# Performance work log

Measured on AMD Instinct MI355X. Metric: run time of the kernel, lower is better.

Reference implementation:

```python
import jax, jax.numpy as jnp
import numpy as np

N_NODES = 100000
N_EDGES = 3200000
IN_CH = 256


def setup_inputs() -> dict:
    key = jax.random.key(0)
    ks = jax.random.split(key, 8)
    x = jax.random.normal(ks[0], (N_NODES, IN_CH), dtype=jnp.float32)
    edge_index = jax.random.randint(ks[1], (2, N_EDGES), 0, N_NODES, dtype=jnp.int64)
    alpha = jnp.ones((), dtype=jnp.float32)
    beta = jnp.ones((), dtype=jnp.float32)
    s = 1.0 / np.sqrt(IN_CH)
    W_mlp = jax.random.normal(ks[2], (1, IN_CH), dtype=jnp.float32) * s
    W_lin = jax.random.normal(ks[3], (1, IN_CH), dtype=jnp.float32) * s
    W_gcn = jax.random.normal(ks[4], (1, IN_CH), dtype=jnp.float32) * s
    W_att = jax.random.normal(ks[5], (3, 3), dtype=jnp.float32) * (1.0 / np.sqrt(3))
    b_att = jax.random.normal(ks[6], (3,), dtype=jnp.float32) * 0.1
    return {"x": x, "edge_index": edge_index, "alpha": alpha, "beta": beta,
            "W_mlp": W_mlp, "W_lin": W_lin, "W_gcn": W_gcn,
            "W_att": W_att, "b_att": b_att}


def _gcn_conv(x, edge_index, W_gcn, num_nodes):
    # PyG GCNConv: add self-loops, symmetric normalization, no bias.
    loop = jnp.arange(num_nodes, dtype=edge_index.dtype)
    row = jnp.concatenate([edge_index[0], loop])  # source
    col = jnp.concatenate([edge_index[1], loop])  # target
    deg = jax.ops.segment_sum(jnp.ones_like(col, dtype=x.dtype), col,
                              num_segments=num_nodes)
    dinv = jnp.where(deg > 0, jax.lax.rsqrt(deg), 0.0)
    norm = dinv[row] * dinv[col]                  # [E+N]
    xw = x @ W_gcn.T                               # [N, 1]
    msg = norm[:, None] * xw[row]                  # [E+N, 1]
    return jax.ops.segment_sum(msg, col, num_segments=num_nodes)  # [N, 1]


def reference(x, edge_index, alpha, beta, W_mlp, W_lin, W_gcn, W_att, b_att):
    num_nodes = x.shape[0]
    # score1: in-degree based
    deg = jax.ops.segment_sum(jnp.ones((edge_index.shape[1],), dtype=x.dtype),
                              edge_index[1], num_segments=num_nodes)
    score1 = jax.nn.sigmoid(alpha * jnp.sqrt(deg) + beta)           # [N]
    # score2: tiny MLP
    score2 = jax.nn.sigmoid((x @ W_mlp.T)[:, 0])                    # [N]
    # score3: GCNConv + linear
    gcn_out = _gcn_conv(x, edge_index, W_gcn, num_nodes)            # [N,1]
    score3 = jax.nn.sigmoid((gcn_out + x @ W_lin.T)[:, 0])          # [N]
    scores = jnp.stack([score1, score2, score3], axis=1)            # [N,3]
    weight = jax.nn.softmax(scores @ W_att.T + b_att, axis=1)       # [N,3]
    fitness = jnp.sum(weight * scores, axis=1)                      # [N]
    return fitness
```

## Files before the change

### kernel.cpp

```cpp
#include <hip/hip_runtime.h>
#include <math.h>

#define N_CH    256
#define SBSHIFT 11
#define SBN     2048
#define NSMAX   64
#define CH      4096
#define EPB_H   16384
#define NCHMAX  1024

__device__ __forceinline__ float sigmoidf_(float v) {
    return 1.0f / (1.0f + expf(-v));
}

__global__ __launch_bounds__(256) void dots_hist_kernel(
    const float* __restrict__ x,
    const float* __restrict__ Wmlp, const float* __restrict__ Wlin,
    const float* __restrict__ Wgcn, const int* __restrict__ dst,
    float* __restrict__ s2dot, float* __restrict__ s3lin, float* __restrict__ xw,
    int* __restrict__ H1,
    int n_nodes, int n_edges, int ns, int nch, int histBlocks)
{
    __shared__ int h1[4][NSMAX];
    if ((int)blockIdx.x < histBlocks) {
        for (int i = threadIdx.x; i < 4 * NSMAX; i += 256) ((int*)h1)[i] = 0;
        __syncthreads();
        int start = blockIdx.x * EPB_H;
        for (int k = 0; k < 4; ++k) {
            for (int m = 0; m < 4; ++m) {
                int e = start + k * CH + (m * 256 + (int)threadIdx.x) * 4;
                if (e + 3 < n_edges) {
                    int4 d4 = *(const int4*)(dst + e);
                    atomicAdd(&h1[k][d4.x >> SBSHIFT], 1);
                    atomicAdd(&h1[k][d4.y >> SBSHIFT], 1);
                    atomicAdd(&h1[k][d4.z >> SBSHIFT], 1);
                    atomicAdd(&h1[k][d4.w >> SBSHIFT], 1);
                } else {
                    for (int ee = e; ee < n_edges && ee >= 0; ++ee)
                        atomicAdd(&h1[k][dst[ee] >> SBSHIFT], 1);
                }
            }
        }
        __syncthreads();
        int k  = threadIdx.x >> 6;
        int sb = threadIdx.x & 63;
        int chunk = blockIdx.x * 4 + k;
        if (sb < ns && chunk < nch)
            H1[(size_t)sb * nch + chunk] = h1[k][sb];
        return;
    }

    int wid  = ((int)blockIdx.x - histBlocks) * 4 + ((int)threadIdx.x >> 6);
    int lane = threadIdx.x & 63;
    if (wid >= n_nodes) return;

    const float4* xr = (const float4*)(x + (size_t)wid * N_CH);
    float4 v  = xr[lane];
    float4 wm = ((const float4*)Wmlp)[lane];
    float4 wl = ((const float4*)Wlin)[lane];
    float4 wg = ((const float4*)Wgcn)[lane];

    float d0 = v.x*wm.x + v.y*wm.y + v.z*wm.z + v.w*wm.w;
    float d1 = v.x*wl.x + v.y*wl.y + v.z*wl.z + v.w*wl.w;
    float d2 = v.x*wg.x + v.y*wg.y + v.z*wg.z + v.w*wg.w;

    #pragma unroll
    for (int off = 32; off; off >>= 1) {
        d0 += __shfl_down(d0, off, 64);
        d1 += __shfl_down(d1, off, 64);
        d2 += __shfl_down(d2, off, 64);
    }
    if (lane == 0) { s2dot[wid] = d0; s3lin[wid] = d1; xw[wid] = d2; }
}

__global__ __launch_bounds__(1024) void scanA_kernel(
    const int* __restrict__ H1, int* __restrict__ O, int* __restrict__ sbT,
    int nch)
{
    __shared__ int s[1024];
    int sb = blockIdx.x, t = threadIdx.x;
    int v = (t < nch) ? H1[(size_t)sb * nch + t] : 0;
    s[t] = v;
    __syncthreads();
    for (int off = 1; off < 1024; off <<= 1) {
        int a = s[t];
        int b = (t >= off) ? s[t - off] : 0;
        __syncthreads();
        s[t] = a + b;
        __syncthreads();
    }
    if (t < nch) O[(size_t)sb * nch + t] = s[t] - v;
    if (t == 1023) sbT[sb] = s[1023];
}

__global__ __launch_bounds__(256) void scanB_kernel(
    const int* __restrict__ sbT,
    int* __restrict__ sbs, int* __restrict__ cstart,
    int* __restrict__ chunkBase, int* __restrict__ chunkLen,
    int ns)
{
    __shared__ int sbsL[NSMAX + 1], nchL[NSMAX], cstL[NSMAX + 1];
    int t = threadIdx.x;
    if (t == 0) {
        int run = 0;
        for (int i = 0; i < ns; ++i) { sbsL[i] = run; run += sbT[i]; }
        sbsL[ns] = run;
        int c = 0;
        for (int i = 0; i < ns; ++i) {
            cstL[i] = c;
            int len = sbsL[i + 1] - sbsL[i];
            nchL[i] = (len + CH - 1) / CH;
            c += nchL[i];
        }
        cstL[ns] = c;
    }
    __syncthreads();
    if (t <= ns) { sbs[t] = sbsL[t]; cstart[t] = cstL[t]; }
    for (int i = t; i < NCHMAX; i += 256) chunkLen[i] = 0;
    __syncthreads();
    for (int sb = 0; sb < ns; ++sb) {
        int n = nchL[sb], base = sbsL[sb], cs = cstL[sb];
        int len = sbsL[sb + 1] - sbsL[sb];
        for (int i = t; i < n; i += 256) {
            chunkBase[cs + i] = base + i * CH;
            chunkLen[cs + i]  = min(CH, len - i * CH);
        }
    }
}

__global__ __launch_bounds__(256) void scatter1_kernel(
    const int* __restrict__ src, const int* __restrict__ dst,
    const int* __restrict__ sbs, const int* __restrict__ O,
    int* __restrict__ cpack, int n_edges, int ns, int nch)
{
    __shared__ int pos0[NSMAX];
    __shared__ int h[NSMAX];
    int c = blockIdx.x;
    if (threadIdx.x < NSMAX) {
        h[threadIdx.x] = 0;
        if (threadIdx.x < (unsigned)ns)
            pos0[threadIdx.x] = sbs[threadIdx.x] + O[(size_t)threadIdx.x * nch + c];
    }
    __syncthreads();
    int start = c * CH;
    for (int m = 0; m < 4; ++m) {
        int e = start + (m * 256 + (int)threadIdx.x) * 4;
        if (e + 3 < n_edges) {
            int4 s4 = *(const int4*)(src + e);
            int4 d4 = *(const int4*)(dst + e);
            int ss[4] = {s4.x, s4.y, s4.z, s4.w};
            int dd[4] = {d4.x, d4.y, d4.z, d4.w};
            #pragma unroll
            for (int j = 0; j < 4; ++j) {
                int sb = dd[j] >> SBSHIFT;
                int r = atomicAdd(&h[sb], 1);
                cpack[pos0[sb] + r] = ss[j] | ((dd[j] & (SBN - 1)) << 17);
            }
        } else {
            for (int ee = e; ee < n_edges && ee >= 0; ++ee) {
                int d = dst[ee];
                int sb = d >> SBSHIFT;
                int r = atomicAdd(&h[sb], 1);
                cpack[pos0[sb] + r] = src[ee] | ((d & (SBN - 1)) << 17);
            }
        }
    }
}

__global__ __launch_bounds__(256) void chunkDeg_kernel(
    const int* __restrict__ cpack, const int* __restrict__ chunkBase,
    const int* __restrict__ chunkLen, int* __restrict__ partialD)
{
    __shared__ int cnt[SBN];
    int c = blockIdx.x;
    int len = chunkLen[c];
    for (int i = threadIdx.x; i < SBN; i += 256) cnt[i] = 0;
    __syncthreads();
    if (len > 0) {
        int base = chunkBase[c];
        for (int e = threadIdx.x; e < len; e += 256)
            atomicAdd(&cnt[cpack[base + e] >> 17], 1);
    }
    __syncthreads();
    if (len > 0) {
        int* row = partialD + (size_t)c * SBN;
        for (int i = threadIdx.x; i < SBN; i += 256) row[i] = cnt[i];
    }
}

__global__ __launch_bounds__(256) void reduceDeg_kernel(
    const int* __restrict__ partialD, const int* __restrict__ cstart,
    const float* __restrict__ xw,
    float* __restrict__ degf, float* __restrict__ dinv, float* __restrict__ sxw,
    int n_nodes)
{
    int i = blockIdx.x * 256 + threadIdx.x;
    if (i >= n_nodes) return;
    int sb = i >> SBSHIFT, li = i & (SBN - 1);
    int c0 = cstart[sb], c1 = cstart[sb + 1];
    int d = 0;
    for (int c = c0; c < c1; ++c) d += partialD[(size_t)c * SBN + li];
    float df = (float)d;
    degf[i] = df;
    float di = rsqrtf(df + 1.0f);
    dinv[i] = di;
    sxw[i]  = di * xw[i];
}

__global__ __launch_bounds__(256) void chunkAcc_kernel(
    const int* __restrict__ cpack, const int* __restrict__ chunkBase,
    const int* __restrict__ chunkLen, const float* __restrict__ sxw,
    float* __restrict__ partialF)
{
    __shared__ float facc[SBN];
    int c = blockIdx.x;
    int len = chunkLen[c];
    for (int i = threadIdx.x; i < SBN; i += 256) facc[i] = 0.0f;
    __syncthreads();
    if (len > 0) {
        int base = chunkBase[c];
        for (int e = threadIdx.x; e < len; e += 256) {
            int w = cpack[base + e];
            atomicAdd(&facc[w >> 17], sxw[w & 0x1FFFF]);
        }
    }
    __syncthreads();
    if (len > 0) {
        float* row = partialF + (size_t)c * SBN;
        for (int i = threadIdx.x; i < SBN; i += 256) row[i] = facc[i];
    }
}

__global__ __launch_bounds__(256) void reduceFinal_kernel(
    const float* __restrict__ partialF, const int* __restrict__ cstart,
    const float* __restrict__ degf, const float* __restrict__ dinv,
    const float* __restrict__ xw, const float* __restrict__ s2dot,
    const float* __restrict__ s3lin,
    const float* __restrict__ alpha, const float* __restrict__ beta,
    const float* __restrict__ Watt, const float* __restrict__ batt,
    float* __restrict__ out, int n_nodes)
{
    int i = blockIdx.x * 256 + threadIdx.x;
    if (i >= n_nodes) return;
    int sb = i >> SBSHIFT, li = i & (SBN - 1);
    int c0 = cstart[sb], c1 = cstart[sb + 1];
    float acc = 0.0f;
    for (int c = c0; c < c1; ++c) acc += partialF[(size_t)c * SBN + li];

    float dn = dinv[i];
    float g  = acc * dn + dn * dn * xw[i];
    float s1 = sigmoidf_(alpha[0] * sqrtf(degf[i]) + beta[0]);
    float s2 = sigmoidf_(s2dot[i]);
    float s3 = sigmoidf_(g + s3lin[i]);

    float z0 = Watt[0]*s1 + Watt[1]*s2 + Watt[2]*s3 + batt[0];
    float z1 = Watt[3]*s1 + Watt[4]*s2 + Watt[5]*s3 + batt[1];
    float z2 = Watt[6]*s1 + Watt[7]*s2 + Watt[8]*s3 + batt[2];

    float m  = fmaxf(z0, fmaxf(z1, z2));
    float e0 = expf(z0 - m), e1 = expf(z1 - m), e2 = expf(z2 - m);
    float inv = 1.0f / (e0 + e1 + e2);
    out[i] = (e0 * s1 + e1 * s2 + e2 * s3) * inv;
}

extern "C" void kernel_launch(void* const* d_in, const int* in_sizes, int n_in,
                              void* d_out, int out_size, void* d_ws, size_t ws_size,
                              hipStream_t stream) {
    const float* x     = (const float*)d_in[0];
    const int*   ei    = (const int*)d_in[1];
    const float* alpha = (const float*)d_in[2];
    const float* beta  = (const float*)d_in[3];
    const float* Wmlp  = (const float*)d_in[4];
    const float* Wlin  = (const float*)d_in[5];
    const float* Wgcn  = (const float*)d_in[6];
    const float* Watt  = (const float*)d_in[7];
    const float* batt  = (const float*)d_in[8];
    float* out = (float*)d_out;

    int n_nodes = in_sizes[0] / N_CH;
    int n_edges = in_sizes[1] / 2;
    const int* src = ei;
    const int* dst = ei + n_edges;

    int ns  = (n_nodes + SBN - 1) >> SBSHIFT;
    int nch = (n_edges + CH - 1) / CH;
    int histBlocks = (n_edges + EPB_H - 1) / EPB_H;
    int maxChunks  = nch + ns;

    size_t off = 0;
    int*   cpack     = (int*)d_ws;          off += (((size_t)n_edges + 1023) & ~(size_t)1023);
    int*   H1        = (int*)d_ws + off;    off += (((size_t)ns * nch + 1023) & ~(size_t)1023);
    int*   O         = (int*)d_ws + off;    off += (((size_t)ns * nch + 1023) & ~(size_t)1023);
    int*   sbT       = (int*)d_ws + off;    off += 128;
    int*   sbs       = (int*)d_ws + off;    off += 128;
    int*   cstart    = (int*)d_ws + off;    off += 128;
    int*   chunkBase = (int*)d_ws + off;    off += NCHMAX;
    int*   chunkLen  = (int*)d_ws + off;    off += NCHMAX;
    int*   partialD  = (int*)d_ws + off;    off += (size_t)maxChunks * SBN;
    float* partialF  = (float*)d_ws + off;  off += (size_t)maxChunks * SBN;
    float* s2dot     = (float*)d_ws + off;  off += (((size_t)n_nodes + 1023) & ~(size_t)1023);
    float* s3lin     = (float*)d_ws + off;  off += (((size_t)n_nodes + 1023) & ~(size_t)1023);
    float* xw        = (float*)d_ws + off;  off += (((size_t)n_nodes + 1023) & ~(size_t)1023);
    float* degf      = (float*)d_ws + off;  off += (((size_t)n_nodes + 1023) & ~(size_t)1023);
    float* dinv      = (float*)d_ws + off;  off += (((size_t)n_nodes + 1023) & ~(size_t)1023);
    float* sxw       = (float*)d_ws + off;  off += (((size_t)n_nodes + 1023) & ~(size_t)1023);

    int dotsBlocks = (n_nodes + 3) / 4;
    dots_hist_kernel<<<histBlocks + dotsBlocks, 256, 0, stream>>>(
        x, Wmlp, Wlin, Wgcn, dst, s2dot, s3lin, xw, H1,
        n_nodes, n_edges, ns, nch, histBlocks);

    scanA_kernel<<<ns, 1024, 0, stream>>>(H1, O, sbT, nch);

    scanB_kernel<<<1, 256, 0, stream>>>(sbT, sbs, cstart, chunkBase, chunkLen, ns);

    scatter1_kernel<<<nch, 256, 0, stream>>>(src, dst, sbs, O, cpack,
                                             n_edges, ns, nch);

    chunkDeg_kernel<<<maxChunks, 256, 0, stream>>>(cpack, chunkBase, chunkLen,
                                                   partialD);

    reduceDeg_kernel<<<(n_nodes + 255) / 256, 256, 0, stream>>>(
        partialD, cstart, xw, degf, dinv, sxw, n_nodes);

    chunkAcc_kernel<<<maxChunks, 256, 0, stream>>>(cpack, chunkBase, chunkLen,
                                                   sxw, partialF);

    reduceFinal_kernel<<<(n_nodes + 255) / 256, 256, 0, stream>>>(
        partialF, cstart, degf, dinv, xw, s2dot, s3lin,
        alpha, beta, Watt, batt, out, n_nodes);
}
```

Before: 255.1 us.

## Stage scatter through shared-memory local sort and drop the scanB kernel

The scatter kernel now sorts each 4096-edge chunk by super-bucket in shared memory first, then writes each bucket's run to the packed array as contiguous writes. This replaces per-edge random global stores. The single-block scanB kernel is removed: every consumer kernel rebuilds the small prefix and chunk tables in shared memory from sbT with one thread, and locates its chunk by binary search. The histogram pass now uses one block per chunk instead of four chunks per block, and the degree and accumulate kernels read with int4 loads. The cost is a serial table build in thread 0 of every block, extra shared memory and barriers in scatter, and more histogram blocks.

```diff
diff --git a/kernel.cpp b/kernel.cpp
--- a/kernel.cpp
+++ b/kernel.cpp
@@ -6,11 +6,25 @@
 #define SBN     2048
 #define NSMAX   64
 #define CH      4096
-#define EPB_H   16384
-#define NCHMAX  1024
 
 __device__ __forceinline__ float sigmoidf_(float v) {
     return 1.0f / (1.0f + expf(-v));
+}
+
+__device__ __forceinline__ void build_tables(const int* sbT, int ns,
+                                             int* sbsL, int* cstL) {
+    if (threadIdx.x == 0) {
+        int run = 0, c = 0;
+        for (int i = 0; i < ns; ++i) {
+            sbsL[i] = run;
+            cstL[i] = c;
+            int len = sbT[i];
+            run += len;
+            c += (len + CH - 1) / CH;
+        }
+        sbsL[ns] = run;
+        cstL[ns] = c;
+    }
 }
 
 __global__ __launch_bounds__(256) void dots_hist_kernel(
@@ -19,38 +33,35 @@
     const float* __restrict__ Wgcn, const int* __restrict__ dst,
     float* __restrict__ s2dot, float* __restrict__ s3lin, float* __restrict__ xw,
     int* __restrict__ H1,
-    int n_nodes, int n_edges, int ns, int nch, int histBlocks)
-{
-    __shared__ int h1[4][NSMAX];
-    if ((int)blockIdx.x < histBlocks) {
-        for (int i = threadIdx.x; i < 4 * NSMAX; i += 256) ((int*)h1)[i] = 0;
+    int n_nodes, int n_edges, int ns, int nch)
+{
+    __shared__ int h[NSMAX];
+    if ((int)blockIdx.x < nch) {
+        int c = blockIdx.x;
+        if (threadIdx.x < NSMAX) h[threadIdx.x] = 0;
         __syncthreads();
-        int start = blockIdx.x * EPB_H;
-        for (int k = 0; k < 4; ++k) {
-            for (int m = 0; m < 4; ++m) {
-                int e = start + k * CH + (m * 256 + (int)threadIdx.x) * 4;
-                if (e + 3 < n_edges) {
-                    int4 d4 = *(const int4*)(dst + e);
-                    atomicAdd(&h1[k][d4.x >> SBSHIFT], 1);
-                    atomicAdd(&h1[k][d4.y >> SBSHIFT], 1);
-                    atomicAdd(&h1[k][d4.z >> SBSHIFT], 1);
-                    atomicAdd(&h1[k][d4.w >> SBSHIFT], 1);
-                } else {
-                    for (int ee = e; ee < n_edges && ee >= 0; ++ee)
-                        atomicAdd(&h1[k][dst[ee] >> SBSHIFT], 1);
-                }
+        int start = c * CH;
+        #pragma unroll
+        for (int m = 0; m < 4; ++m) {
+            int e = start + (m * 256 + (int)threadIdx.x) * 4;
+            if (e + 3 < n_edges) {
+                int4 d4 = *(const int4*)(dst + e);
+                atomicAdd(&h[d4.x >> SBSHIFT], 1);
+                atomicAdd(&h[d4.y >> SBSHIFT], 1);
+                atomicAdd(&h[d4.z >> SBSHIFT], 1);
+                atomicAdd(&h[d4.w >> SBSHIFT], 1);
+            } else {
+                for (int ee = e; ee < n_edges && ee >= 0; ++ee)
+                    atomicAdd(&h[dst[ee] >> SBSHIFT], 1);
             }
         }
         __syncthreads();
-        int k  = threadIdx.x >> 6;
-        int sb = threadIdx.x & 63;
-        int chunk = blockIdx.x * 4 + k;
-        if (sb < ns && chunk < nch)
-            H1[(size_t)sb * nch + chunk] = h1[k][sb];
+        if (threadIdx.x < (unsigned)ns)
+            H1[(size_t)threadIdx.x * nch + c] = h[threadIdx.x];
         return;
     }
 
-    int wid  = ((int)blockIdx.x - histBlocks) * 4 + ((int)threadIdx.x >> 6);
+    int wid  = ((int)blockIdx.x - nch) * 4 + ((int)threadIdx.x >> 6);
     int lane = threadIdx.x & 63;
     if (wid >= n_nodes) return;
 
@@ -93,111 +104,130 @@
     if (t == 1023) sbT[sb] = s[1023];
 }
 
-__global__ __launch_bounds__(256) void scanB_kernel(
-    const int* __restrict__ sbT,
-    int* __restrict__ sbs, int* __restrict__ cstart,
-    int* __restrict__ chunkBase, int* __restrict__ chunkLen,
-    int ns)
-{
-    __shared__ int sbsL[NSMAX + 1], nchL[NSMAX], cstL[NSMAX + 1];
-    int t = threadIdx.x;
-    if (t == 0) {
-        int run = 0;
-        for (int i = 0; i < ns; ++i) { sbsL[i] = run; run += sbT[i]; }
-        sbsL[ns] = run;
-        int c = 0;
-        for (int i = 0; i < ns; ++i) {
-            cstL[i] = c;
-            int len = sbsL[i + 1] - sbsL[i];
-            nchL[i] = (len + CH - 1) / CH;
-            c += nchL[i];
-        }
-        cstL[ns] = c;
-    }
-    __syncthreads();
-    if (t <= ns) { sbs[t] = sbsL[t]; cstart[t] = cstL[t]; }
-    for (int i = t; i < NCHMAX; i += 256) chunkLen[i] = 0;
-    __syncthreads();
-    for (int sb = 0; sb < ns; ++sb) {
-        int n = nchL[sb], base = sbsL[sb], cs = cstL[sb];
-        int len = sbsL[sb + 1] - sbsL[sb];
-        for (int i = t; i < n; i += 256) {
-            chunkBase[cs + i] = base + i * CH;
-            chunkLen[cs + i]  = min(CH, len - i * CH);
-        }
-    }
-}
-
-__global__ __launch_bounds__(256) void scatter1_kernel(
+__global__ __launch_bounds__(256) void scatter_kernel(
     const int* __restrict__ src, const int* __restrict__ dst,
-    const int* __restrict__ sbs, const int* __restrict__ O,
+    const int* __restrict__ sbT, const int* __restrict__ O,
     int* __restrict__ cpack, int n_edges, int ns, int nch)
 {
+    __shared__ int sbsL[NSMAX + 1], cstL[NSMAX + 1];
     __shared__ int pos0[NSMAX];
+    __shared__ int lp[NSMAX + 1];
     __shared__ int h[NSMAX];
+    __shared__ int sorted[CH];
+
     int c = blockIdx.x;
-    if (threadIdx.x < NSMAX) {
-        h[threadIdx.x] = 0;
-        if (threadIdx.x < (unsigned)ns)
-            pos0[threadIdx.x] = sbs[threadIdx.x] + O[(size_t)threadIdx.x * nch + c];
-    }
-    __syncthreads();
+    build_tables(sbT, ns, sbsL, cstL);
+    if (threadIdx.x < NSMAX) h[threadIdx.x] = 0;
+    __syncthreads();
+    if (threadIdx.x < (unsigned)ns)
+        pos0[threadIdx.x] = sbsL[threadIdx.x] + O[(size_t)threadIdx.x * nch + c];
+
     int start = c * CH;
+    int cnt = n_edges - start; if (cnt > CH) cnt = CH;
+
+    int4 s4[4], d4[4];
+    #pragma unroll
     for (int m = 0; m < 4; ++m) {
         int e = start + (m * 256 + (int)threadIdx.x) * 4;
         if (e + 3 < n_edges) {
-            int4 s4 = *(const int4*)(src + e);
-            int4 d4 = *(const int4*)(dst + e);
-            int ss[4] = {s4.x, s4.y, s4.z, s4.w};
-            int dd[4] = {d4.x, d4.y, d4.z, d4.w};
-            #pragma unroll
+            s4[m] = *(const int4*)(src + e);
+            d4[m] = *(const int4*)(dst + e);
+            atomicAdd(&h[d4[m].x >> SBSHIFT], 1);
+            atomicAdd(&h[d4[m].y >> SBSHIFT], 1);
+            atomicAdd(&h[d4[m].z >> SBSHIFT], 1);
+            atomicAdd(&h[d4[m].w >> SBSHIFT], 1);
+        } else {
+            s4[m] = make_int4(-1, -1, -1, -1);
+            int* sp = (int*)&s4[m]; int* dp = (int*)&d4[m];
             for (int j = 0; j < 4; ++j) {
-                int sb = dd[j] >> SBSHIFT;
-                int r = atomicAdd(&h[sb], 1);
-                cpack[pos0[sb] + r] = ss[j] | ((dd[j] & (SBN - 1)) << 17);
+                int ee = e + j;
+                if (ee < n_edges && ee >= 0) {
+                    sp[j] = src[ee]; dp[j] = dst[ee];
+                    atomicAdd(&h[dp[j] >> SBSHIFT], 1);
+                }
             }
-        } else {
-            for (int ee = e; ee < n_edges && ee >= 0; ++ee) {
-                int d = dst[ee];
+        }
+    }
+    __syncthreads();
+    if (threadIdx.x == 0) {
+        int run = 0;
+        for (int i = 0; i < ns; ++i) { lp[i] = run; run += h[i]; }
+        lp[ns] = run;
+    }
+    __syncthreads();
+    if (threadIdx.x < NSMAX) h[threadIdx.x] = 0;
+    __syncthreads();
+    #pragma unroll
+    for (int m = 0; m < 4; ++m) {
+        int* sp = (int*)&s4[m]; int* dp = (int*)&d4[m];
+        #pragma unroll
+        for (int j = 0; j < 4; ++j) {
+            if (sp[j] >= 0) {
+                int d = dp[j];
                 int sb = d >> SBSHIFT;
                 int r = atomicAdd(&h[sb], 1);
-                cpack[pos0[sb] + r] = src[ee] | ((d & (SBN - 1)) << 17);
+                sorted[lp[sb] + r] = sp[j] | ((d & (SBN - 1)) << 17);
             }
         }
     }
+    __syncthreads();
+    for (int p = threadIdx.x; p < cnt; p += 256) {
+        int lo = 0, hi = ns;
+        while (hi - lo > 1) { int mid = (lo + hi) >> 1; if (lp[mid] <= p) lo = mid; else hi = mid; }
+        cpack[pos0[lo] + (p - lp[lo])] = sorted[p];
+    }
 }
 
 __global__ __launch_bounds__(256) void chunkDeg_kernel(
-    const int* __restrict__ cpack, const int* __restrict__ chunkBase,
-    const int* __restrict__ chunkLen, int* __restrict__ partialD)
-{
+    const int* __restrict__ cpack, const int* __restrict__ sbT,
+    int* __restrict__ partialD, int ns)
+{
+    __shared__ int sbsL[NSMAX + 1], cstL[NSMAX + 1];
     __shared__ int cnt[SBN];
+    build_tables(sbT, ns, sbsL, cstL);
+    for (int i = threadIdx.x; i < SBN; i += 256) cnt[i] = 0;
+    __syncthreads();
     int c = blockIdx.x;
-    int len = chunkLen[c];
-    for (int i = threadIdx.x; i < SBN; i += 256) cnt[i] = 0;
-    __syncthreads();
-    if (len > 0) {
-        int base = chunkBase[c];
-        for (int e = threadIdx.x; e < len; e += 256)
-            atomicAdd(&cnt[cpack[base + e] >> 17], 1);
-    }
-    __syncthreads();
-    if (len > 0) {
-        int* row = partialD + (size_t)c * SBN;
-        for (int i = threadIdx.x; i < SBN; i += 256) row[i] = cnt[i];
-    }
+    if (c >= cstL[ns]) return;
+    int lo = 0, hi = ns;
+    while (hi - lo > 1) { int mid = (lo + hi) >> 1; if (cstL[mid] <= c) lo = mid; else hi = mid; }
+    int sb = lo;
+    int i0 = c - cstL[sb];
+    int base = sbsL[sb] + i0 * CH;
+    int len = sbsL[sb + 1] - base; if (len > CH) len = CH;
+
+    #pragma unroll
+    for (int m = 0; m < 4; ++m) {
+        int e = (m * 256 + (int)threadIdx.x) * 4;
+        if (e + 3 < len) {
+            int4 w4 = *(const int4*)(cpack + base + e);
+            atomicAdd(&cnt[w4.x >> 17], 1);
+            atomicAdd(&cnt[w4.y >> 17], 1);
+            atomicAdd(&cnt[w4.z >> 17], 1);
+            atomicAdd(&cnt[w4.w >> 17], 1);
+        } else {
+            for (int ee = e; ee < len && ee >= 0; ++ee)
+                atomicAdd(&cnt[cpack[base + ee] >> 17], 1);
+        }
+    }
+    __syncthreads();
+    int* row = partialD + (size_t)c * SBN;
+    for (int i = threadIdx.x; i < SBN; i += 256) row[i] = cnt[i];
 }
 
 __global__ __launch_bounds__(256) void reduceDeg_kernel(
-    const int* __restrict__ partialD, const int* __restrict__ cstart,
+    const int* __restrict__ partialD, const int* __restrict__ sbT,
     const float* __restrict__ xw,
     float* __restrict__ degf, float* __restrict__ dinv, float* __restrict__ sxw,
-    int n_nodes)
-{
+    int n_nodes, int ns)
+{
+    __shared__ int sbsL[NSMAX + 1], cstL[NSMAX + 1];
+    build_tables(sbT, ns, sbsL, cstL);
+    __syncthreads();
     int i = blockIdx.x * 256 + threadIdx.x;
     if (i >= n_nodes) return;
     int sb = i >> SBSHIFT, li = i & (SBN - 1);
-    int c0 = cstart[sb], c1 = cstart[sb + 1];
+    int c0 = cstL[sb], c1 = cstL[sb + 1];
     int d = 0;
     for (int c = c0; c < c1; ++c) d += partialD[(size_t)c * SBN + li];
     float df = (float)d;
@@ -208,42 +238,60 @@
 }
 
 __global__ __launch_bounds__(256) void chunkAcc_kernel(
-    const int* __restrict__ cpack, const int* __restrict__ chunkBase,
-    const int* __restrict__ chunkLen, const float* __restrict__ sxw,
-    float* __restrict__ partialF)
-{
+    const int* __restrict__ cpack, const int* __restrict__ sbT,
+    const float* __restrict__ sxw, float* __restrict__ partialF, int ns)
+{
+    __shared__ int sbsL[NSMAX + 1], cstL[NSMAX + 1];
     __shared__ float facc[SBN];
+    build_tables(sbT, ns, sbsL, cstL);
+    for (int i = threadIdx.x; i < SBN; i += 256) facc[i] = 0.0f;
+    __syncthreads();
     int c = blockIdx.x;
-    int len = chunkLen[c];
-    for (int i = threadIdx.x; i < SBN; i += 256) facc[i] = 0.0f;
-    __syncthreads();
-    if (len > 0) {
-        int base = chunkBase[c];
-        for (int e = threadIdx.x; e < len; e += 256) {
-            int w = cpack[base + e];
-            atomicAdd(&facc[w >> 17], sxw[w & 0x1FFFF]);
-        }
-    }
-    __syncthreads();
-    if (len > 0) {
-        float* row = partialF + (size_t)c * SBN;
-        for (int i = threadIdx.x; i < SBN; i += 256) row[i] = facc[i];
-    }
+    if (c >= cstL[ns]) return;
+    int lo = 0, hi = ns;
+    while (hi - lo > 1) { int mid = (lo + hi) >> 1; if (cstL[mid] <= c) lo = mid; else hi = mid; }
+    int sb = lo;
+    int i0 = c - cstL[sb];
+    int base = sbsL[sb] + i0 * CH;
+    int len = sbsL[sb + 1] - base; if (len > CH) len = CH;
+
+    #pragma unroll
+    for (int m = 0; m < 4; ++m) {
+        int e = (m * 256 + (int)threadIdx.x) * 4;
+        if (e + 3 < len) {
+            int4 w4 = *(const int4*)(cpack + base + e);
+            atomicAdd(&facc[w4.x >> 17], sxw[w4.x & 0x1FFFF]);
+            atomicAdd(&facc[w4.y >> 17], sxw[w4.y & 0x1FFFF]);
+            atomicAdd(&facc[w4.z >> 17], sxw[w4.z & 0x1FFFF]);
+            atomicAdd(&facc[w4.w >> 17], sxw[w4.w & 0x1FFFF]);
+        } else {
+            for (int ee = e; ee < len && ee >= 0; ++ee) {
+                int w = cpack[base + ee];
+                atomicAdd(&facc[w >> 17], sxw[w & 0x1FFFF]);
+            }
+        }
+    }
+    __syncthreads();
+    float* row = partialF + (size_t)c * SBN;
+    for (int i = threadIdx.x; i < SBN; i += 256) row[i] = facc[i];
 }
 
 __global__ __launch_bounds__(256) void reduceFinal_kernel(
-    const float* __restrict__ partialF, const int* __restrict__ cstart,
+    const float* __restrict__ partialF, const int* __restrict__ sbT,
     const float* __restrict__ degf, const float* __restrict__ dinv,
     const float* __restrict__ xw, const float* __restrict__ s2dot,
     const float* __restrict__ s3lin,
     const float* __restrict__ alpha, const float* __restrict__ beta,
     const float* __restrict__ Watt, const float* __restrict__ batt,
-    float* __restrict__ out, int n_nodes)
-{
+    float* __restrict__ out, int n_nodes, int ns)
+{
+    __shared__ int sbsL[NSMAX + 1], cstL[NSMAX + 1];
+    build_tables(sbT, ns, sbsL, cstL);
+    __syncthreads();
     int i = blockIdx.x * 256 + threadIdx.x;
     if (i >= n_nodes) return;
     int sb = i >> SBSHIFT, li = i & (SBN - 1);
-    int c0 = cstart[sb], c1 = cstart[sb + 1];
+    int c0 = cstL[sb], c1 = cstL[sb + 1];
     float acc = 0.0f;
     for (int c = c0; c < c1; ++c) acc += partialF[(size_t)c * SBN + li];
 
@@ -284,49 +332,40 @@
 
     int ns  = (n_nodes + SBN - 1) >> SBSHIFT;
     int nch = (n_edges + CH - 1) / CH;
-    int histBlocks = (n_edges + EPB_H - 1) / EPB_H;
-    int maxChunks  = nch + ns;
+    int maxChunks = nch + ns;
 
     size_t off = 0;
-    int*   cpack     = (int*)d_ws;          off += (((size_t)n_edges + 1023) & ~(size_t)1023);
-    int*   H1        = (int*)d_ws + off;    off += (((size_t)ns * nch + 1023) & ~(size_t)1023);
-    int*   O         = (int*)d_ws + off;    off += (((size_t)ns * nch + 1023) & ~(size_t)1023);
-    int*   sbT       = (int*)d_ws + off;    off += 128;
-    int*   sbs       = (int*)d_ws + off;    off += 128;
-    int*   cstart    = (int*)d_ws + off;    off += 128;
-    int*   chunkBase = (int*)d_ws + off;    off += NCHMAX;
-    int*   chunkLen  = (int*)d_ws + off;    off += NCHMAX;
-    int*   partialD  = (int*)d_ws + off;    off += (size_t)maxChunks * SBN;
-    float* partialF  = (float*)d_ws + off;  off += (size_t)maxChunks * SBN;
-    float* s2dot     = (float*)d_ws + off;  off += (((size_t)n_nodes + 1023) & ~(size_t)1023);
-    float* s3lin     = (float*)d_ws + off;  off += (((size_t)n_nodes + 1023) & ~(size_t)1023);
-    float* xw        = (float*)d_ws + off;  off += (((size_t)n_nodes + 1023) & ~(size_t)1023);
-    float* degf      = (float*)d_ws + off;  off += (((size_t)n_nodes + 1023) & ~(size_t)1023);
-    float* dinv      = (float*)d_ws + off;  off += (((size_t)n_nodes + 1023) & ~(size_t)1023);
-    float* sxw       = (float*)d_ws + off;  off += (((size_t)n_nodes + 1023) & ~(size_t)1023);
+    int*   cpack    = (int*)d_ws;          off += (((size_t)n_edges + 1023) & ~(size_t)1023);
+    int*   H1       = (int*)d_ws + off;    off += (((size_t)ns * nch + 1023) & ~(size_t)1023);
+    int*   O        = (int*)d_ws + off;    off += (((size_t)ns * nch + 1023) & ~(size_t)1023);
+    int*   sbT      = (int*)d_ws + off;    off += 128;
+    int*   partialD = (int*)d_ws + off;    off += (size_t)maxChunks * SBN;
+    float* partialF = (float*)d_ws + off;  off += (size_t)maxChunks * SBN;
+    float* s2dot    = (float*)d_ws + off;  off += (((size_t)n_nodes + 1023) & ~(size_t)1023);
+    float* s3lin    = (float*)d_ws + off;  off += (((size_t)n_nodes + 1023) & ~(size_t)1023);
+    float* xw       = (float*)d_ws + off;  off += (((size_t)n_nodes + 1023) & ~(size_t)1023);
+    float* degf     = (float*)d_ws + off;  off += (((size_t)n_nodes + 1023) & ~(size_t)1023);
+    float* dinv     = (float*)d_ws + off;  off += (((size_t)n_nodes + 1023) & ~(size_t)1023);
+    float* sxw      = (float*)d_ws + off;  off += (((size_t)n_nodes + 1023) & ~(size_t)1023);
 
     int dotsBlocks = (n_nodes + 3) / 4;
-    dots_hist_kernel<<<histBlocks + dotsBlocks, 256, 0, stream>>>(
+    dots_hist_kernel<<<nch + dotsBlocks, 256, 0, stream>>>(
         x, Wmlp, Wlin, Wgcn, dst, s2dot, s3lin, xw, H1,
-        n_nodes, n_edges, ns, nch, histBlocks);
+        n_nodes, n_edges, ns, nch);
 
     scanA_kernel<<<ns, 1024, 0, stream>>>(H1, O, sbT, nch);
 
-    scanB_kernel<<<1, 256, 0, stream>>>(sbT, sbs, cstart, chunkBase, chunkLen, ns);
-
-    scatter1_kernel<<<nch, 256, 0, stream>>>(src, dst, sbs, O, cpack,
-                                             n_edges, ns, nch);
-
-    chunkDeg_kernel<<<maxChunks, 256, 0, stream>>>(cpack, chunkBase, chunkLen,
-                                                   partialD);
+    scatter_kernel<<<nch, 256, 0, stream>>>(src, dst, sbT, O, cpack,
+                                            n_edges, ns, nch);
+
+    chunkDeg_kernel<<<maxChunks, 256, 0, stream>>>(cpack, sbT, partialD, ns);
 
     reduceDeg_kernel<<<(n_nodes + 255) / 256, 256, 0, stream>>>(
-        partialD, cstart, xw, degf, dinv, sxw, n_nodes);
-
-    chunkAcc_kernel<<<maxChunks, 256, 0, stream>>>(cpack, chunkBase, chunkLen,
-                                                   sxw, partialF);
+        partialD, sbT, xw, degf, dinv, sxw, n_nodes, ns);
+
+    chunkAcc_kernel<<<maxChunks, 256, 0, stream>>>(cpack, sbT, sxw, partialF, ns);
 
     reduceFinal_kernel<<<(n_nodes + 255) / 256, 256, 0, stream>>>(
-        partialF, cstart, degf, dinv, xw, s2dot, s3lin,
-        alpha, beta, Watt, batt, out, n_nodes);
-}
+        partialF, sbT, degf, dinv, xw, s2dot, s3lin,
+        alpha, beta, Watt, batt, out, n_nodes, ns);
+}
```

New measurement: 244.5 us. 1.04x faster.
